# Kernel optimization log

Hardware: AMD Instinct MI355X
Metric: run time of the kernel (lower is better)

Reference implementation:

```python
import jax, jax.numpy as jnp
import numpy as np
import math

B, L, CIN = 16, 1024, 14
T = 256            # num_tokens
H = 2 * T          # S4 channel width
N = 32             # S4 state size (d_state)
E = 128            # embedding_dim
DEPTH = 6
BETA0, BETA1 = 1e-4, 2e-2


def conv1x1(W, b, x):
    # W: [O, C], b: [O], x: [B, C, L] -> [B, O, L]
    return jnp.einsum('oc,bcl->bol', W, x) + b[None, :, None]


def layernorm_c(x, g, b):
    # normalize over channel dim of [B, C, L]
    mu = jnp.mean(x, axis=1, keepdims=True)
    var = jnp.mean((x - mu) ** 2, axis=1, keepdims=True)
    return (x - mu) * jax.lax.rsqrt(var + 1e-5) * g[None, :, None] + b[None, :, None]


def s4d(u, log_dt, logA_re, A_im, C_re, C_im, D):
    # Standard S4D: diagonal SSM, ZOH-ish discretization, FFT depthwise conv.
    # u: [B, H, L]
    Lq = u.shape[-1]
    dt = jnp.exp(log_dt)                       # [H]
    A = -jnp.exp(logA_re) + 1j * A_im          # [H, N]
    dtA = A * dt[:, None]                      # [H, N]
    C = (C_re + 1j * C_im) * (jnp.exp(dtA) - 1.0) / A
    V = jnp.exp(dtA[:, :, None] * jnp.arange(Lq, dtype=jnp.float32))  # [H, N, L]
    K = 2.0 * jnp.einsum('hn,hnl->hl', C, V).real                    # [H, L]
    nfft = 2 * Lq
    y = jnp.fft.irfft(jnp.fft.rfft(u, n=nfft) * jnp.fft.rfft(K, n=nfft)[None], n=nfft)[..., :Lq]
    return y + D[None, :, None] * u


def setup_inputs() -> dict:
    key = jax.random.key(0)
    ks = iter(jax.random.split(key, 64))
    nrm = lambda shape, s=1.0: jax.random.normal(next(ks), shape, jnp.float32) * s
    inp = {}
    inp['x'] = nrm((B, L, CIN))
    inp['t'] = jax.random.uniform(next(ks), (B,), jnp.float32, 1e-3, 1.0)
    # diffusion embedding
    inp['gfp_W'] = nrm((E // 2,), 30.0)
    inp['emb_w1'] = nrm((E, E), E ** -0.5); inp['emb_b1'] = jnp.zeros((E,), jnp.float32)
    inp['emb_w2'] = nrm((E, E), E ** -0.5); inp['emb_b2'] = jnp.zeros((E,), jnp.float32)
    # top-level projections
    inp['in_w'] = nrm((T, CIN), CIN ** -0.5); inp['in_b'] = jnp.zeros((T,), jnp.float32)
    inp['out1_w'] = nrm((T, T), T ** -0.5); inp['out1_b'] = jnp.zeros((T,), jnp.float32)
    inp['out2_w'] = nrm((CIN, T), T ** -0.5); inp['out2_b'] = jnp.zeros((CIN,), jnp.float32)
    # per-block params (stacked over depth)
    inp['dp_w'] = nrm((DEPTH, T, E), E ** -0.5); inp['dp_b'] = jnp.zeros((DEPTH, T), jnp.float32)
    inp['ip_w'] = nrm((DEPTH, H, T), T ** -0.5); inp['ip_b'] = jnp.zeros((DEPTH, H), jnp.float32)
    inp['op_w'] = nrm((DEPTH, H, T), T ** -0.5); inp['op_b'] = jnp.zeros((DEPTH, H), jnp.float32)
    # S4D params: [DEPTH, 2, H, ...] (two S4 layers per block)
    lo, hi = math.log(1e-3), math.log(1e-1)
    inp['s4_log_dt'] = jax.random.uniform(next(ks), (DEPTH, 2, H), jnp.float32, lo, hi)
    inp['s4_logA_re'] = jnp.full((DEPTH, 2, H, N), math.log(0.5), jnp.float32)
    inp['s4_A_im'] = jnp.broadcast_to(math.pi * jnp.arange(N, dtype=jnp.float32), (DEPTH, 2, H, N)).copy()
    inp['s4_C_re'] = nrm((DEPTH, 2, H, N), 0.5 ** 0.5)
    inp['s4_C_im'] = nrm((DEPTH, 2, H, N), 0.5 ** 0.5)
    inp['s4_D'] = nrm((DEPTH, 2, H))
    inp['ln_g'] = jnp.ones((DEPTH, 2, H), jnp.float32)
    inp['ln_b'] = jnp.zeros((DEPTH, 2, H), jnp.float32)
    return inp


def reference(x, t, gfp_W, emb_w1, emb_b1, emb_w2, emb_b2, in_w, in_b,
              out1_w, out1_b, out2_w, out2_b, dp_w, dp_b, ip_w, ip_b,
              op_w, op_b, s4_log_dt, s4_logA_re, s4_A_im, s4_C_re, s4_C_im,
              s4_D, ln_g, ln_b):
    xt = jnp.swapaxes(x, -1, -2)  # [B, CIN, L]
    # Gaussian Fourier projection + MLP (SiLU)
    xp = t[:, None] * gfp_W[None, :] * (2.0 * math.pi)
    emb = jnp.concatenate([jnp.sin(xp), jnp.cos(xp)], axis=-1)        # [B, E]
    emb = jax.nn.silu(emb @ emb_w1.T + emb_b1)
    emb = jax.nn.silu(emb @ emb_w2.T + emb_b2)
    h = conv1x1(in_w, in_b, xt)                                       # [B, T, L]
    skip_sum = jnp.zeros_like(h)
    for d in range(DEPTH):
        y = h + (emb @ dp_w[d].T + dp_b[d])[:, :, None]
        y = conv1x1(ip_w[d], ip_b[d], y)                              # [B, H, L]
        y = s4d(y, s4_log_dt[d, 0], s4_logA_re[d, 0], s4_A_im[d, 0], s4_C_re[d, 0], s4_C_im[d, 0], s4_D[d, 0])
        y = layernorm_c(y, ln_g[d, 0], ln_b[d, 0])
        y = s4d(y, s4_log_dt[d, 1], s4_logA_re[d, 1], s4_A_im[d, 1], s4_C_re[d, 1], s4_C_im[d, 1], s4_D[d, 1])
        y = layernorm_c(y, ln_g[d, 1], ln_b[d, 1])
        gate, filt = jnp.split(y, 2, axis=1)
        y = jax.nn.sigmoid(gate) * jnp.tanh(filt)                     # [B, T, L]
        y = conv1x1(op_w[d], op_b[d], y)                              # [B, H, L]
        res, skip = jnp.split(y, 2, axis=1)
        h = (h + res) / math.sqrt(2.0)
        skip_sum = skip_sum + skip
    z = skip_sum / math.sqrt(float(DEPTH))
    z = jax.nn.relu(conv1x1(out1_w, out1_b, z))
    z = conv1x1(out2_w, out2_b, z)                                    # [B, CIN, L]
    beta = BETA0 + t * (BETA1 - BETA0)                                # linear schedule
    z = z / jnp.sqrt(beta)[:, None, None]
    return jnp.swapaxes(z, -1, -2)                                    # [B, L, CIN]
```

## Files before the change

### kernel.cpp

```cpp
#include <hip/hip_runtime.h>

#define BB     16
#define LLEN   1024
#define CINN   14
#define TSZ    256
#define HSZ    512
#define NST    32
#define ESZ    128
#define NDEPTH 6
#define QHN    (HSZ*NST)

#define RS2 0.70710678118654752f
#define IS6 0.40824829046386302f

typedef unsigned short u16;
typedef unsigned int   u32;
typedef _Float16 f16;
typedef __attribute__((ext_vector_type(2)))  _Float16 f16x2;
typedef __attribute__((ext_vector_type(4)))  _Float16 f16x4;
typedef __attribute__((ext_vector_type(8)))  _Float16 f16x8;
typedef __attribute__((ext_vector_type(16))) float    f32x16;

#define OFF_WIP   0u
#define OFF_WOP   393216u
#define OFF_LAMP  786432u
#define OFF_WO1   1181696u
#define OFF_BB    1214464u
#define OFF_Y16   5388288u
#define OFF_HT    9582592u
#define OFF_GT    11679744u
#define OFF_ST    13776896u
#define OFF_ZT    15874048u
#define OFF_MEAN  17971200u
#define OFF_RSTD  17987584u
#define OFF_MATS  18003968u
#define WS_FLOATS 55752704u

#define MATS_PER_LAYER ((size_t)512*12288)

__device__ __forceinline__ void gload_lds16(const void* g, void* l){
  __builtin_amdgcn_global_load_lds(
      (const __attribute__((address_space(1))) unsigned int*)g,
      (__attribute__((address_space(3))) unsigned int*)(unsigned int)(unsigned long long)l,
      16, 0, 0);
}

__device__ __forceinline__ size_t swz_idx(int b, int l, int g){
  return ((((size_t)b*4 + (g>>3))*1024 + l)*8 + ((g&7) ^ (l&7)))*8;
}

__global__ __launch_bounds__(256) void build_kernel(const float* __restrict__ log_dt,
                                                    const float* __restrict__ logA,
                                                    const float* __restrict__ Aim,
                                                    const float* __restrict__ Cre,
                                                    const float* __restrict__ Cim,
                                                    const float* __restrict__ Dd,
                                                    float2* __restrict__ lamP,
                                                    f16* __restrict__ mats){
  __shared__ float Pre[65][33];
  __shared__ float Pim[65][33];
  __shared__ float Kk[64];
  __shared__ float Kpart[4][64];
  __shared__ float2 Lm[32];
  __shared__ float2 Cc[32];
  int bid = blockIdx.x;
  int q   = bid >> 9;
  int h   = bid & 511;
  int tid = threadIdx.x;
  if (tid < 32){
    int n = tid;
    int gid = q*QHN + h*NST + n;
    float dt  = expf(log_dt[q*HSZ + h]);
    float are = -expf(logA[gid]);
    float aim = Aim[gid];
    float dre = are*dt, dim = aim*dt;
    float e   = expf(dre);
    float lre = e*cosf(dim), lim = e*sinf(dim);
    float nre = lre - 1.f, nim = lim;
    float invden = 1.f/(are*are + aim*aim);
    float tre = (nre*are + nim*aim)*invden;
    float tim = (nim*are - nre*aim)*invden;
    float cr = Cre[gid], ci = Cim[gid];
    Lm[n] = make_float2(lre, lim);
    Cc[n] = make_float2(2.f*(cr*tre - ci*tim), 2.f*(cr*tim + ci*tre));
    float pr = lre, pi = lim;
#pragma unroll
    for (int i=0;i<6;i++){ float t2 = pr*pr - pi*pi; pi = 2.f*pr*pi; pr = t2; }
    lamP[gid] = make_float2(pr, pi);
  }
  __syncthreads();
  int n  = tid & 31;
  int pg = tid >> 5;
  {
    float2 l = Lm[n];
    float ar=l.x, ai=l.y;
#pragma unroll
    for (int i=0;i<3;i++){ float t2 = ar*ar - ai*ai; ai = 2.f*ar*ai; ar = t2; }
    float br=1.f, bi=0.f;
    for (int i=0;i<pg;i++){ float t2 = br*ar - bi*ai; bi = br*ai + bi*ar; br = t2; }
    float pr=br, pi=bi;
#pragma unroll
    for (int i=0;i<8;i++){
      Pre[8*pg+i][n] = pr; Pim[8*pg+i][n] = pi;
      float t2 = pr*l.x - pi*l.y; pi = pr*l.y + pi*l.x; pr = t2;
    }
    if (pg == 7){ Pre[64][n] = pr; Pim[64][n] = pi; }
  }
  __syncthreads();
  {
    int m = tid & 63, p2 = tid >> 6;
    float s = 0.f;
#pragma unroll
    for (int n2=p2*8; n2<p2*8+8; n2++){
      float2 c_ = Cc[n2];
      s += c_.x*Pre[m][n2] - c_.y*Pim[m][n2];
    }
    Kpart[p2][m] = s;
  }
  __syncthreads();
  if (tid < 64) Kk[tid] = Kpart[0][tid]+Kpart[1][tid]+Kpart[2][tid]+Kpart[3][tid];
  __syncthreads();
  float Kdiag = Kk[0] + Dd[q*HSZ + h];
  f16* base = mats + (size_t)bid*12288;
#pragma unroll
  for (int jj=0; jj<6; jj++){
    int job = jj*256 + tid;
    int mat = job >> 9;
    int rem = job & 511;
    int m = rem & 63;
    int g = rem >> 6;
    f16x8 vals;
    if (mat == 0){
#pragma unroll
      for (int j8=0;j8<8;j8++){
        int k = g*8 + j8;
        float v = (m > k) ? Kk[m-k] : ((m == k) ? Kdiag : 0.f);
        vals[j8] = (f16)v;
      }
    } else if (mat == 1){
      int n2 = m >> 1; int im = m & 1;
#pragma unroll
      for (int j8=0;j8<8;j8++){
        int k = g*8 + j8; int p = 63 - k;
        vals[j8] = (f16)(im ? Pim[p][n2] : Pre[p][n2]);
      }
    } else {
#pragma unroll
      for (int j8=0;j8<8;j8++){
        int k = g*8 + j8; int n2 = k >> 1;
        float2 c_ = Cc[n2];
        float pr = Pre[m+1][n2], pi = Pim[m+1][n2];
        float re  = c_.x*pr - c_.y*pi;
        float imv = c_.x*pi + c_.y*pr;
        vals[j8] = (f16)((k & 1) ? -imv : re);
      }
    }
    *(f16x8*)(base + mat*4096 + (g*64 + m)*8) = vals;
  }
}

__global__ __launch_bounds__(256) void embdpe_bb(const float* __restrict__ t, const float* __restrict__ gw,
                                                 const float* __restrict__ w1, const float* __restrict__ b1,
                                                 const float* __restrict__ w2, const float* __restrict__ b2,
                                                 const float* __restrict__ dw, const float* __restrict__ db,
                                                 const float* __restrict__ ipw, const float* __restrict__ ipb,
                                                 float* __restrict__ bbp){
  __shared__ float e0[128], e1[128], e2[128];
  __shared__ float dpe[256];
  int bid = blockIdx.x;
  int d = bid >> 4, b = bid & 15;
  int tid = threadIdx.x;
  float tb = t[b];
  if (tid < 64){
    float xp = tb * gw[tid] * 6.283185307179586f;
    e0[tid]    = sinf(xp);
    e0[tid+64] = cosf(xp);
  }
  __syncthreads();
  if (tid < 128){
    float a = b1[tid];
    const float* wr = w1 + tid*128;
    for (int i=0;i<128;i++) a = fmaf(e0[i], wr[i], a);
    e1[tid] = a / (1.f + __expf(-a));
  }
  __syncthreads();
  if (tid < 128){
    float a2 = b2[tid];
    const float* wr = w2 + tid*128;
    for (int i=0;i<128;i++) a2 = fmaf(e1[i], wr[i], a2);
    e2[tid] = a2 / (1.f + __expf(-a2));
  }
  __syncthreads();
  {
    const float* wp = dw + (size_t)(d*TSZ + tid)*ESZ;
    float a = db[d*TSZ + tid];
    for (int e=0;e<128;e++) a = fmaf(e2[e], wp[e], a);
    dpe[tid] = a;
  }
  __syncthreads();
#pragma unroll
  for (int r=0;r<2;r++){
    int m = r*256 + tid;
    const float* wp = ipw + (size_t)(d*HSZ + m)*TSZ;
    float a = ipb[d*HSZ + m];
    for (int e=0;e<256;e++) a = fmaf(dpe[e], wp[e], a);
    bbp[(size_t)(d*BB + b)*HSZ + m] = a;
  }
}

__global__ __launch_bounds__(256) void prep_wts(const float* __restrict__ x,  const float* __restrict__ inw,
                                                const float* __restrict__ inb,
                                                const float* __restrict__ ipw, const float* __restrict__ opw,
                                                const float* __restrict__ o1w,
                                                f16* __restrict__ WfIP, f16* __restrict__ WfOP,
                                                f16* __restrict__ WfO1, f16* __restrict__ hT){
  __shared__ __align__(16) char SMEM[49152];
  int bid = blockIdx.x;
  int tid = threadIdx.x;
  if (bid < 256){
    float* ws  = (float*)SMEM;
    float* bs2 = (float*)(SMEM + 14336);
    f16*  TT   = (f16*)(SMEM + 15360);
#pragma unroll
    for (int c=0;c<14;c++) ws[tid*14+c] = inw[tid*14+c];
    bs2[tid] = inb[tid];
    __syncthreads();
    int b  = bid >> 4;
    int l0 = (bid & 15) * 64;
    int ll = tid & 63;
    int tq = tid >> 6;
    float xv[14];
    const float* xp = x + (size_t)(b*LLEN + l0 + ll)*CINN;
#pragma unroll
    for (int c=0;c<14;c++) xv[c] = xp[c];
    for (int tt=tq*64; tt<tq*64+64; tt++){
      float a = bs2[tt];
#pragma unroll
      for (int c=0;c<14;c++) a = fmaf(ws[tt*14+c], xv[c], a);
      TT[ll*264 + tt] = (f16)a;
    }
    __syncthreads();
#pragma unroll
    for (int i=0;i<8;i++){
      int job = i*256 + tid;
      int l2 = job >> 5, gi = job & 31;
      f16x8 hv = *(const f16x8*)(TT + l2*264 + gi*8);
      *(f16x8*)(hT + swz_idx(b, l0 + l2, gi)) = hv;
    }
  } else {
    int gid = (bid - 256)*256 + tid;
    const float* src; f16* dst; float scale = 1.f;
    if (gid < 98304){
      int d = gid >> 14, rem = gid & 16383, r = rem >> 5, g = rem & 31;
      src = ipw + ((size_t)(d*512 + r))*256 + g*8;
      dst = WfIP + (size_t)d*131072 + (((g>>3)*512 + r)*8 + ((g&7)^(r&7)))*8;
    } else if (gid < 196608){
      int g2 = gid - 98304;
      int d = g2 >> 14, rem = g2 & 16383, r = rem >> 5, g = rem & 31;
      src = opw + ((size_t)(d*512 + r))*256 + g*8;
      dst = WfOP + (size_t)d*131072 + (((g>>3)*512 + r)*8 + ((g&7)^(r&7)))*8;
    } else {
      int g3 = gid - 196608;
      int r = g3 >> 5, g = g3 & 31;
      src = o1w + (size_t)r*256 + g*8;
      dst = WfO1 + (((g>>3)*256 + r)*8 + ((g&7)^(r&7)))*8;
      scale = IS6;
    }
    float4 u0 = *(const float4*)src;
    float4 u1 = *(const float4*)(src+4);
    f16x8 hv;
    hv[0]=(f16)(u0.x*scale); hv[1]=(f16)(u0.y*scale); hv[2]=(f16)(u0.z*scale); hv[3]=(f16)(u0.w*scale);
    hv[4]=(f16)(u1.x*scale); hv[5]=(f16)(u1.y*scale); hv[6]=(f16)(u1.z*scale); hv[7]=(f16)(u1.w*scale);
    *(f16x8*)dst = hv;
  }
}

template<int MODE>
__global__ __launch_bounds__(256) void gemm_k(const f16* __restrict__ Wf, const float* __restrict__ bias,
                                              const f16* __restrict__ XT,
                                              f16* __restrict__ Y16o,
                                              f16* __restrict__ hT16, f16* __restrict__ sT16, int first){
  __shared__ __align__(16) f16 sm[17408];
  f16* As = sm;
  f16* Bs = sm + 8192;
  int tid = threadIdx.x;
  int lane = tid & 63;
  int wv = tid >> 6;
  int n_blk = blockIdx.x * 128;
  int m_blk = blockIdx.y * 128;
  int bz = blockIdx.z;
  const int M = (MODE==2) ? 256 : 512;
  int wm = (wv & 1) * 64;
  int wn = (wv >> 1) * 64;

  f32x16 acc[2][2];
#pragma unroll
  for (int mi=0;mi<2;mi++)
#pragma unroll
    for (int ni=0;ni<2;ni++)
#pragma unroll
      for (int r=0;r<16;r++) acc[mi][ni][r] = 0.f;

  for (int kt=0; kt<4; kt++){
    const f16* asrc = Wf + ((size_t)kt*M + m_blk)*64 + tid*8;
    const f16* bsrc = XT + ((size_t)(bz*4 + kt)*1024 + n_blk)*64 + tid*8;
#pragma unroll
    for (int i=0;i<4;i++){
      gload_lds16(asrc + i*2048, As + (i*256 + wv*64)*8);
      gload_lds16(bsrc + i*2048, Bs + (i*256 + wv*64)*8);
    }
    __syncthreads();
#pragma unroll
    for (int ks=0; ks<4; ks++){
      int q = lane >> 5;
      int gk = ks*2 + q;
      f16x8 af[2], bf[2];
#pragma unroll
      for (int mi=0; mi<2; mi++){
        int m = wm + mi*32 + (lane & 31);
        af[mi] = *(const f16x8*)(As + (m*8 + (gk ^ (m&7)))*8);
      }
#pragma unroll
      for (int ni=0; ni<2; ni++){
        int n = wn + ni*32 + (lane & 31);
        bf[ni] = *(const f16x8*)(Bs + (n*8 + (gk ^ (n&7)))*8);
      }
#pragma unroll
      for (int mi=0; mi<2; mi++)
#pragma unroll
        for (int ni=0; ni<2; ni++)
          acc[mi][ni] = __builtin_amdgcn_mfma_f32_32x32x16_f16(af[mi], bf[ni], acc[mi][ni], 0, 0, 0);
    }
    __syncthreads();
  }

  int q = lane >> 5;
  if (MODE == 0){
#pragma unroll
    for (int mi=0;mi<2;mi++)
#pragma unroll
      for (int ni=0;ni<2;ni++){
        int col_l = wn + ni*32 + (lane & 31);
#pragma unroll
        for (int r=0;r<16;r++){
          int row_l = wm + mi*32 + (r&3) + 8*(r>>2) + 4*q;
          float v = acc[mi][ni][r] + bias[bz*HSZ + m_blk + row_l];
          sm[row_l*136 + col_l] = (f16)v;
        }
      }
    __syncthreads();
#pragma unroll
    for (int i=0;i<8;i++){
      int job = i*256 + tid;
      int rr = job >> 4, c8 = job & 15;
      f16x8 hv = *(const f16x8*)(sm + rr*136 + c8*8);
      *(f16x8*)(Y16o + ((size_t)bz*HSZ + m_blk + rr)*LLEN + n_blk + c8*8) = hv;
    }
  } else if (MODE == 2){
#pragma unroll
    for (int mi=0;mi<2;mi++)
#pragma unroll
      for (int ni=0;ni<2;ni++){
        int col_l = wn + ni*32 + (lane & 31);
#pragma unroll
        for (int r=0;r<16;r++){
          int row_l = wm + mi*32 + (r&3) + 8*(r>>2) + 4*q;
          float v = fmaxf(acc[mi][ni][r] + bias[m_blk + row_l], 0.f);
          sm[col_l*136 + row_l] = (f16)v;
        }
      }
    __syncthreads();
#pragma unroll
    for (int i=0;i<8;i++){
      int job = i*256 + tid;
      int n = job >> 4, m8 = job & 15;
      f16x8 hv = *(const f16x8*)(sm + n*136 + m8*8);
      *(f16x8*)(Y16o + ((size_t)bz*LLEN + n_blk + n)*TSZ + m_blk + m8*8) = hv;
    }
  } else {
    int isRes = (blockIdx.y < 2);
    f16* dst = isRes ? hT16 : sT16;
    int gbase = isRes ? (m_blk >> 3) : ((m_blk - TSZ) >> 3);
    int doLoad = isRes || !first;
    if (doLoad){
#pragma unroll
      for (int i=0;i<8;i++){
        int job = i*256 + tid;
        int n = job >> 4, m8 = job & 15;
        f16x8 hv = *(const f16x8*)(dst + swz_idx(bz, n_blk + n, gbase + m8));
        *(f16x8*)(sm + n*136 + m8*8) = hv;
      }
      __syncthreads();
    }
#pragma unroll
    for (int mi=0;mi<2;mi++)
#pragma unroll
      for (int ni=0;ni<2;ni++){
        int col_l = wn + ni*32 + (lane & 31);
#pragma unroll
        for (int r=0;r<16;r++){
          int row_l = wm + mi*32 + (r&3) + 8*(r>>2) + 4*q;
          float v = acc[mi][ni][r] + bias[m_blk + row_l];
          if (isRes){
            float old = (float)sm[col_l*136 + row_l];
            sm[col_l*136 + row_l] = (f16)((old + v)*RS2);
          } else if (first){
            sm[col_l*136 + row_l] = (f16)v;
          } else {
            float old = (float)sm[col_l*136 + row_l];
            sm[col_l*136 + row_l] = (f16)(old + v);
          }
        }
      }
    __syncthreads();
#pragma unroll
    for (int i=0;i<8;i++){
      int job = i*256 + tid;
      int n = job >> 4, m8 = job & 15;
      f16x8 hv = *(const f16x8*)(sm + n*136 + m8*8);
      *(f16x8*)(dst + swz_idx(bz, n_blk + n, gbase + m8)) = hv;
    }
  }
}

template<int LN>
__global__ __launch_bounds__(128) void s4_mfma(const f16* __restrict__ matsq,
                                               const float2* __restrict__ lamPq,
                                               const f16* u, f16* y,
                                               const float* __restrict__ meanp,
                                               const float* __restrict__ rstdp,
                                               const float* __restrict__ gp,
                                               const float* __restrict__ btp){
  __shared__ f16 Ubuf[64*72];
  __shared__ f16 ZSbuf[64*72];

  int tid  = threadIdx.x;
  int w    = tid >> 6;
  int lane = tid & 63;
  int q    = lane >> 5;
  int colL = lane & 31;
  int h  = blockIdx.x & 511;
  int bq = blockIdx.x >> 9;
  int b0 = bq*4;

  float gv = 0.f, bv = 0.f;
  if (LN){ gv = gp[h]; bv = btp[h]; }

  const f16* matT = matsq + (size_t)h*12288;
  const f16* matV = matT + 4096;
  const f16* matE = matT + 8192;

#pragma unroll
  for (int i=0;i<4;i++){
    int fidx = i*64 + lane;
    int row = fidx >> 7;
    int l   = (fidx & 127)*8;
    int b   = b0 + 2*w + row;
    f16x8 hv = *(const f16x8*)(u + ((size_t)b*HSZ + h)*LLEN + l);
    if (LN){
      float4 m0 = *(const float4*)(meanp + b*LLEN + l);
      float4 m1 = *(const float4*)(meanp + b*LLEN + l + 4);
      float4 r0 = *(const float4*)(rstdp + b*LLEN + l);
      float4 r1 = *(const float4*)(rstdp + b*LLEN + l + 4);
      float mm[8] = {m0.x,m0.y,m0.z,m0.w,m1.x,m1.y,m1.z,m1.w};
      float rr[8] = {r0.x,r0.y,r0.z,r0.w,r1.x,r1.y,r1.z,r1.w};
#pragma unroll
      for (int e=0;e<8;e++)
        hv[e] = (f16)(((float)hv[e] - mm[e])*rr[e]*gv + bv);
    }
    int col = (2*w + row)*16 + (l >> 6);
    *(f16x8*)(Ubuf + col*72 + (l & 63)) = hv;
  }
  __syncthreads();

  int strip = w*32;

  {
    f32x16 zacc[2];
#pragma unroll
    for (int mt=0;mt<2;mt++)
#pragma unroll
      for (int r=0;r<16;r++) zacc[mt][r] = 0.f;
#pragma unroll
    for (int kt=0; kt<4; kt++){
      int kg = kt*2 + q;
      f16x8 bfrag = *(const f16x8*)(Ubuf + (strip+colL)*72 + kg*8);
#pragma unroll
      for (int mt=0; mt<2; mt++){
        f16x8 afrag = *(const f16x8*)(matV + ((size_t)(kg*64 + mt*32 + colL))*8);
        zacc[mt] = __builtin_amdgcn_mfma_f32_32x32x16_f16(afrag, bfrag, zacc[mt], 0, 0, 0);
      }
    }
#pragma unroll
    for (int mt=0;mt<2;mt++)
#pragma unroll
      for (int rg=0;rg<4;rg++){
        int st0 = mt*32 + rg*8 + q*4;
        f16x4 zp;
        zp[0]=(f16)zacc[mt][rg*4+0]; zp[1]=(f16)zacc[mt][rg*4+1];
        zp[2]=(f16)zacc[mt][rg*4+2]; zp[3]=(f16)zacc[mt][rg*4+3];
        *(f16x4*)(ZSbuf + (strip+colL)*72 + st0) = zp;
      }
  }
  __syncthreads();

  {
    int n  = lane & 31;
    int colb = (2*w + (lane>>5))*16;
    float2 l64 = lamPq[h*NST + n];
    f16x2 zv[16];
#pragma unroll
    for (int c=0;c<16;c++)
      zv[c] = *(f16x2*)(ZSbuf + (colb + c)*72 + 2*n);
    float Sre = 0.f, Sim = 0.f;
#pragma unroll
    for (int c=0;c<16;c++){
      float zr = (float)zv[c][0], zi = (float)zv[c][1];
      f16x2 sp_; sp_[0] = (f16)Sre; sp_[1] = (f16)Sim;
      zv[c] = sp_;
      float nr = fmaf(l64.x, Sre, fmaf(-l64.y, Sim, zr));
      float ni = fmaf(l64.x, Sim, fmaf( l64.y, Sre, zi));
      Sre = nr; Sim = ni;
    }
#pragma unroll
    for (int c=0;c<16;c++)
      *(f16x2*)(ZSbuf + (colb + c)*72 + 2*n) = zv[c];
  }
  __syncthreads();

  f32x16 yacc[2];
#pragma unroll
  for (int mt=0;mt<2;mt++)
#pragma unroll
    for (int r=0;r<16;r++) yacc[mt][r] = 0.f;
#pragma unroll
  for (int kt=0; kt<4; kt++){
    int kg = kt*2 + q;
    f16x8 bu = *(const f16x8*)(Ubuf  + (strip+colL)*72 + kg*8);
    f16x8 bs = *(const f16x8*)(ZSbuf + (strip+colL)*72 + kg*8);
#pragma unroll
    for (int mt=0; mt<2; mt++){
      f16x8 aT = *(const f16x8*)(matT + ((size_t)(kg*64 + mt*32 + colL))*8);
      yacc[mt] = __builtin_amdgcn_mfma_f32_32x32x16_f16(aT, bu, yacc[mt], 0, 0, 0);
    }
#pragma unroll
    for (int mt=0; mt<2; mt++){
      f16x8 aE = *(const f16x8*)(matE + ((size_t)(kg*64 + mt*32 + colL))*8);
      yacc[mt] = __builtin_amdgcn_mfma_f32_32x32x16_f16(aE, bs, yacc[mt], 0, 0, 0);
    }
  }
  __syncthreads();

#pragma unroll
  for (int mt=0;mt<2;mt++)
#pragma unroll
    for (int rg=0;rg<4;rg++){
      int j0 = mt*32 + rg*8 + q*4;
      f16x4 yv;
      yv[0]=(f16)yacc[mt][rg*4+0]; yv[1]=(f16)yacc[mt][rg*4+1];
      yv[2]=(f16)yacc[mt][rg*4+2]; yv[3]=(f16)yacc[mt][rg*4+3];
      *(f16x4*)(ZSbuf + (strip+colL)*72 + j0) = yv;
    }
  __syncthreads();
#pragma unroll
  for (int i=0;i<4;i++){
    int fidx = i*64 + lane;
    int row = fidx >> 7;
    int l   = (fidx & 127)*8;
    int b   = b0 + 2*w + row;
    int col = (2*w + row)*16 + (l >> 6);
    f16x8 hv = *(const f16x8*)(ZSbuf + col*72 + (l & 63));
    *(f16x8*)(y + ((size_t)b*HSZ + h)*LLEN + l) = hv;
  }
}

__global__ __launch_bounds__(256) void ln_stats(const f16* __restrict__ in,
                                                float* __restrict__ mean, float* __restrict__ rstd){
  __shared__ float rs[4][32];
  __shared__ float rq[4][32];
  int tid = threadIdx.x;
  int lg = tid & 3;
  int hb = tid >> 2;
  int w  = tid >> 6;
  int b  = blockIdx.x >> 5;
  int l0 = (blockIdx.x & 31) << 5;
  float s8[8], q8[8];
#pragma unroll
  for (int j=0;j<8;j++){ s8[j]=0.f; q8[j]=0.f; }
  const f16* basep = in + (size_t)(b*HSZ)*LLEN + l0 + lg*8;
#pragma unroll
  for (int i=0;i<8;i++){
    int h = hb + 64*i;
    f16x8 hv = *(const f16x8*)(basep + (size_t)h*LLEN);
#pragma unroll
    for (int j=0;j<8;j++){
      float v = (float)hv[j];
      s8[j] += v; q8[j] = fmaf(v,v,q8[j]);
    }
  }
#pragma unroll
  for (int d=4; d<64; d<<=1){
#pragma unroll
    for (int j=0;j<8;j++){
      s8[j] += __shfl_xor(s8[j], (unsigned)d);
      q8[j] += __shfl_xor(q8[j], (unsigned)d);
    }
  }
  if (((tid>>2) & 15) == 0){
#pragma unroll
    for (int j=0;j<8;j++){
      rs[w][lg*8+j] = s8[j];
      rq[w][lg*8+j] = q8[j];
    }
  }
  __syncthreads();
  if (tid < 32){
    float S = rs[0][tid]+rs[1][tid]+rs[2][tid]+rs[3][tid];
    float Q = rq[0][tid]+rq[1][tid]+rq[2][tid]+rq[3][tid];
    float mn = S * (1.f/HSZ);
    float var = Q * (1.f/HSZ) - mn*mn;
    mean[b*LLEN + l0 + tid] = mn;
    rstd[b*LLEN + l0 + tid] = rsqrtf(var + 1e-5f);
  }
}

__global__ __launch_bounds__(256) void ln_gate_kernel(const f16* __restrict__ in, f16* __restrict__ gT,
                                                      const float* __restrict__ g, const float* __restrict__ bt){
  __shared__ float rs[4][32];
  __shared__ float rq[4][32];
  __shared__ float mbuf[32], rbuf[32];
  __shared__ f16 gbuf[32*264];
  int tid = threadIdx.x;
  int lg = tid & 3;
  int w  = tid >> 6;
  int b  = blockIdx.x >> 5;
  int l0 = (blockIdx.x & 31) << 5;
  {
    int hb = tid >> 2;
    float s8[8], q8[8];
#pragma unroll
    for (int j=0;j<8;j++){ s8[j]=0.f; q8[j]=0.f; }
    const f16* basep = in + (size_t)(b*HSZ)*LLEN + l0 + lg*8;
#pragma unroll
    for (int i=0;i<8;i++){
      int h = hb + 64*i;
      f16x8 hv = *(const f16x8*)(basep + (size_t)h*LLEN);
#pragma unroll
      for (int j=0;j<8;j++){
        float v = (float)hv[j];
        s8[j] += v; q8[j] = fmaf(v,v,q8[j]);
      }
    }
#pragma unroll
    for (int d=4; d<64; d<<=1){
#pragma unroll
      for (int j=0;j<8;j++){
        s8[j] += __shfl_xor(s8[j], (unsigned)d);
        q8[j] += __shfl_xor(q8[j], (unsigned)d);
      }
    }
    if (((tid>>2) & 15) == 0){
#pragma unroll
      for (int j=0;j<8;j++){
        rs[w][lg*8+j] = s8[j];
        rq[w][lg*8+j] = q8[j];
      }
    }
  }
  __syncthreads();
  if (tid < 32){
    float S = rs[0][tid]+rs[1][tid]+rs[2][tid]+rs[3][tid];
    float Q = rq[0][tid]+rq[1][tid]+rq[2][tid]+rq[3][tid];
    float mn = S * (1.f/HSZ);
    float var = Q * (1.f/HSZ) - mn*mn;
    mbuf[tid] = mn;
    rbuf[tid] = rsqrtf(var + 1e-5f);
  }
  __syncthreads();
  {
    int tq = tid >> 2;
    float mloc[8], rloc[8];
#pragma unroll
    for (int j=0;j<8;j++){ mloc[j]=mbuf[lg*8+j]; rloc[j]=rbuf[lg*8+j]; }
    const f16* basep = in + (size_t)(b*HSZ)*LLEN + l0 + lg*8;
#pragma unroll
    for (int i=0;i<4;i++){
      int t = tq + 64*i;
      f16x8 av = *(const f16x8*)(basep + (size_t)t*LLEN);
      f16x8 fv = *(const f16x8*)(basep + (size_t)(t+256)*LLEN);
      float ga = g[t], ba = bt[t], gf = g[t+256], bf2 = bt[t+256];
#pragma unroll
      for (int j=0;j<8;j++){
        float a = ((float)av[j] - mloc[j])*rloc[j]*ga + ba;
        float f = ((float)fv[j] - mloc[j])*rloc[j]*gf + bf2;
        float sg = 1.f/(1.f+__expf(-a));
        float th = 1.f - 2.f/(__expf(2.f*f)+1.f);
        gbuf[(lg*8+j)*264 + t] = (f16)(sg*th);
      }
    }
  }
  __syncthreads();
#pragma unroll
  for (int i=0;i<4;i++){
    int job = i*256 + tid;
    int ll = job >> 5, gi = job & 31;
    f16x8 hv = *(const f16x8*)(gbuf + ll*264 + gi*8);
    *(f16x8*)(gT + swz_idx(b, l0 + ll, gi)) = hv;
  }
}

__global__ __launch_bounds__(256) void out2_kernel(const float* __restrict__ w2, const float* __restrict__ b2,
                                                   const float* __restrict__ t, const f16* __restrict__ zT,
                                                   float* __restrict__ outp){
  __shared__ f16 zt[64*264];
  __shared__ float wsm[14*256];
  __shared__ float part[64][4][16];
  __shared__ float bs[14];
  int tid = threadIdx.x;
#pragma unroll
  for (int c=0;c<14;c++) wsm[c*256+tid] = w2[c*256+tid];
  if (tid < 14) bs[tid] = b2[tid];
  int b = blockIdx.x >> 4;
  int l0 = (blockIdx.x & 15) * 64;
#pragma unroll
  for (int i=0;i<8;i++){
    int job = i*256 + tid;
    int ll = job >> 5, g8 = (job & 31)*8;
    f16x8 hv = *(const f16x8*)(zT + ((size_t)b*LLEN + l0 + ll)*TSZ + g8);
    *(f16x8*)(zt + ll*264 + g8) = hv;
  }
  __syncthreads();
  int l = tid >> 2;
  int g = tid & 3;
  float acc[14];
#pragma unroll
  for (int c=0;c<14;c++) acc[c]=0.f;
  for (int k=0;k<64;k++){
    float zv = (float)zt[l*264 + g*64 + k];
#pragma unroll
    for (int c=0;c<14;c++) acc[c] = fmaf(wsm[c*256 + g*64 + k], zv, acc[c]);
  }
#pragma unroll
  for (int c=0;c<14;c++) part[l][g][c] = acc[c];
  __syncthreads();
  if (g == 0){
    float tb = t[b];
    float scale = rsqrtf(1e-4f + tb*(2e-2f - 1e-4f));
    float* op = outp + (size_t)(b*LLEN + l0 + l)*CINN;
#pragma unroll
    for (int c=0;c<14;c++)
      op[c] = (part[l][0][c]+part[l][1][c]+part[l][2][c]+part[l][3][c] + bs[c])*scale;
  }
}

extern "C" void kernel_launch(void* const* d_in, const int* in_sizes, int n_in,
                              void* d_out, int out_size, void* d_ws, size_t ws_size,
                              hipStream_t stream) {
  (void)in_sizes; (void)n_in; (void)out_size;
  if (ws_size < (size_t)WS_FLOATS * 4) return;

  const float* x      = (const float*)d_in[0];
  const float* t      = (const float*)d_in[1];
  const float* gfpW   = (const float*)d_in[2];
  const float* ew1    = (const float*)d_in[3];
  const float* eb1    = (const float*)d_in[4];
  const float* ew2    = (const float*)d_in[5];
  const float* eb2    = (const float*)d_in[6];
  const float* in_w   = (const float*)d_in[7];
  const float* in_b   = (const float*)d_in[8];
  const float* out1_w = (const float*)d_in[9];
  const float* out1_b = (const float*)d_in[10];
  const float* out2_w = (const float*)d_in[11];
  const float* out2_b = (const float*)d_in[12];
  const float* dp_w   = (const float*)d_in[13];
  const float* dp_b   = (const float*)d_in[14];
  const float* ip_w   = (const float*)d_in[15];
  const float* ip_b   = (const float*)d_in[16];
  const float* op_w   = (const float*)d_in[17];
  const float* op_b   = (const float*)d_in[18];
  const float* log_dt = (const float*)d_in[19];
  const float* logA   = (const float*)d_in[20];
  const float* Aim    = (const float*)d_in[21];
  const float* Cre    = (const float*)d_in[22];
  const float* Cim    = (const float*)d_in[23];
  const float* s4D    = (const float*)d_in[24];
  const float* ln_g   = (const float*)d_in[25];
  const float* ln_b   = (const float*)d_in[26];
  float* out = (float*)d_out;
  float* ws = (float*)d_ws;

  f16*    WfIP = (f16*)(ws + OFF_WIP);
  f16*    WfOP = (f16*)(ws + OFF_WOP);
  float2* lamP = (float2*)(ws + OFF_LAMP);
  f16*    WfO1 = (f16*)(ws + OFF_WO1);
  float*  bbp  = ws + OFF_BB;
  f16*    y16  = (f16*)(ws + OFF_Y16);
  f16*    hT16 = (f16*)(ws + OFF_HT);
  f16*    gT16 = (f16*)(ws + OFF_GT);
  f16*    sT16 = (f16*)(ws + OFF_ST);
  f16*    zT16 = (f16*)(ws + OFF_ZT);
  float*  meanb = ws + OFF_MEAN;
  float*  rstdb = ws + OFF_RSTD;
  f16*    mats = (f16*)(ws + OFF_MATS);

  build_kernel<<<6144,256,0,stream>>>(log_dt, logA, Aim, Cre, Cim, s4D, lamP, mats);
  embdpe_bb<<<96,256,0,stream>>>(t, gfpW, ew1, eb1, ew2, eb2, dp_w, dp_b, ip_w, ip_b, bbp);
  prep_wts<<<1056,256,0,stream>>>(x, in_w, in_b, ip_w, op_w, out1_w,
                                  WfIP, WfOP, WfO1, hT16);

  for (int d=0; d<NDEPTH; d++){
    int q0 = d*2, q1 = d*2+1;
    gemm_k<0><<<dim3(8,4,16),256,0,stream>>>(WfIP + (size_t)d*131072, bbp + (size_t)d*BB*HSZ,
                                             hT16, y16, nullptr, nullptr, 0);
    s4_mfma<0><<<2048,128,0,stream>>>(mats + (size_t)q0*MATS_PER_LAYER, lamP + (size_t)q0*QHN,
                                      y16, y16, nullptr, nullptr, nullptr, nullptr);
    ln_stats<<<512,256,0,stream>>>(y16, meanb, rstdb);
    s4_mfma<1><<<2048,128,0,stream>>>(mats + (size_t)q1*MATS_PER_LAYER, lamP + (size_t)q1*QHN,
                                      y16, y16, meanb, rstdb, ln_g + q0*HSZ, ln_b + q0*HSZ);
    ln_gate_kernel<<<512,256,0,stream>>>(y16, gT16, ln_g + q1*HSZ, ln_b + q1*HSZ);
    gemm_k<1><<<dim3(8,4,16),256,0,stream>>>(WfOP + (size_t)d*131072, op_b + d*HSZ,
                                             gT16, nullptr, hT16, sT16, (d==0)?1:0);
  }
  gemm_k<2><<<dim3(8,2,16),256,0,stream>>>(WfO1, out1_b, sT16, zT16, nullptr, nullptr, 0);
  out2_kernel<<<256,256,0,stream>>>(out2_w, out2_b, t, zT16, out);
}
```

Before: 649.8 us.

## Double-buffer GEMM LDS tiles, merge embedding kernel, cache LN input in LDS

```diff
diff --git a/kernel.cpp b/kernel.cpp
--- a/kernel.cpp
+++ b/kernel.cpp
@@ -159,61 +159,18 @@
   }
 }
 
-__global__ __launch_bounds__(256) void embdpe_bb(const float* __restrict__ t, const float* __restrict__ gw,
-                                                 const float* __restrict__ w1, const float* __restrict__ b1,
-                                                 const float* __restrict__ w2, const float* __restrict__ b2,
-                                                 const float* __restrict__ dw, const float* __restrict__ db,
-                                                 const float* __restrict__ ipw, const float* __restrict__ ipb,
-                                                 float* __restrict__ bbp){
-  __shared__ float e0[128], e1[128], e2[128];
-  __shared__ float dpe[256];
-  int bid = blockIdx.x;
-  int d = bid >> 4, b = bid & 15;
-  int tid = threadIdx.x;
-  float tb = t[b];
-  if (tid < 64){
-    float xp = tb * gw[tid] * 6.283185307179586f;
-    e0[tid]    = sinf(xp);
-    e0[tid+64] = cosf(xp);
-  }
-  __syncthreads();
-  if (tid < 128){
-    float a = b1[tid];
-    const float* wr = w1 + tid*128;
-    for (int i=0;i<128;i++) a = fmaf(e0[i], wr[i], a);
-    e1[tid] = a / (1.f + __expf(-a));
-  }
-  __syncthreads();
-  if (tid < 128){
-    float a2 = b2[tid];
-    const float* wr = w2 + tid*128;
-    for (int i=0;i<128;i++) a2 = fmaf(e1[i], wr[i], a2);
-    e2[tid] = a2 / (1.f + __expf(-a2));
-  }
-  __syncthreads();
-  {
-    const float* wp = dw + (size_t)(d*TSZ + tid)*ESZ;
-    float a = db[d*TSZ + tid];
-    for (int e=0;e<128;e++) a = fmaf(e2[e], wp[e], a);
-    dpe[tid] = a;
-  }
-  __syncthreads();
-#pragma unroll
-  for (int r=0;r<2;r++){
-    int m = r*256 + tid;
-    const float* wp = ipw + (size_t)(d*HSZ + m)*TSZ;
-    float a = ipb[d*HSZ + m];
-    for (int e=0;e<256;e++) a = fmaf(dpe[e], wp[e], a);
-    bbp[(size_t)(d*BB + b)*HSZ + m] = a;
-  }
-}
-
 __global__ __launch_bounds__(256) void prep_wts(const float* __restrict__ x,  const float* __restrict__ inw,
                                                 const float* __restrict__ inb,
                                                 const float* __restrict__ ipw, const float* __restrict__ opw,
                                                 const float* __restrict__ o1w,
+                                                const float* __restrict__ t,  const float* __restrict__ gw,
+                                                const float* __restrict__ w1, const float* __restrict__ b1,
+                                                const float* __restrict__ w2, const float* __restrict__ b2,
+                                                const float* __restrict__ dw, const float* __restrict__ db,
+                                                const float* __restrict__ ipb,
                                                 f16* __restrict__ WfIP, f16* __restrict__ WfOP,
-                                                f16* __restrict__ WfO1, f16* __restrict__ hT){
+                                                f16* __restrict__ WfO1, f16* __restrict__ hT,
+                                                float* __restrict__ bbp){
   __shared__ __align__(16) char SMEM[49152];
   int bid = blockIdx.x;
   int tid = threadIdx.x;
@@ -247,7 +204,7 @@
       f16x8 hv = *(const f16x8*)(TT + l2*264 + gi*8);
       *(f16x8*)(hT + swz_idx(b, l0 + l2, gi)) = hv;
     }
-  } else {
+  } else if (bid < 1056){
     int gid = (bid - 256)*256 + tid;
     const float* src; f16* dst; float scale = 1.f;
     if (gid < 98304){
@@ -272,6 +229,49 @@
     hv[0]=(f16)(u0.x*scale); hv[1]=(f16)(u0.y*scale); hv[2]=(f16)(u0.z*scale); hv[3]=(f16)(u0.w*scale);
     hv[4]=(f16)(u1.x*scale); hv[5]=(f16)(u1.y*scale); hv[6]=(f16)(u1.z*scale); hv[7]=(f16)(u1.w*scale);
     *(f16x8*)dst = hv;
+  } else {
+    float* e0  = (float*)SMEM;
+    float* e1  = (float*)(SMEM + 512);
+    float* e2  = (float*)(SMEM + 1024);
+    float* dpe = (float*)(SMEM + 1536);
+    int idx = bid - 1056;
+    int d = idx >> 4, b = idx & 15;
+    float tb = t[b];
+    if (tid < 64){
+      float xp = tb * gw[tid] * 6.283185307179586f;
+      e0[tid]    = sinf(xp);
+      e0[tid+64] = cosf(xp);
+    }
+    __syncthreads();
+    if (tid < 128){
+      float a = b1[tid];
+      const float* wr = w1 + tid*128;
+      for (int i=0;i<128;i++) a = fmaf(e0[i], wr[i], a);
+      e1[tid] = a / (1.f + __expf(-a));
+    }
+    __syncthreads();
+    if (tid < 128){
+      float a2 = b2[tid];
+      const float* wr = w2 + tid*128;
+      for (int i=0;i<128;i++) a2 = fmaf(e1[i], wr[i], a2);
+      e2[tid] = a2 / (1.f + __expf(-a2));
+    }
+    __syncthreads();
+    {
+      const float* wp = dw + (size_t)(d*TSZ + tid)*ESZ;
+      float a = db[d*TSZ + tid];
+      for (int e=0;e<128;e++) a = fmaf(e2[e], wp[e], a);
+      dpe[tid] = a;
+    }
+    __syncthreads();
+#pragma unroll
+    for (int r=0;r<2;r++){
+      int m = r*256 + tid;
+      const float* wp = ipw + (size_t)(d*HSZ + m)*TSZ;
+      float a = ipb[d*HSZ + m];
+      for (int e=0;e<256;e++) a = fmaf(dpe[e], wp[e], a);
+      bbp[(size_t)(d*BB + b)*HSZ + m] = a;
+    }
   }
 }
 
@@ -280,9 +280,7 @@
                                               const f16* __restrict__ XT,
                                               f16* __restrict__ Y16o,
                                               f16* __restrict__ hT16, f16* __restrict__ sT16, int first){
-  __shared__ __align__(16) f16 sm[17408];
-  f16* As = sm;
-  f16* Bs = sm + 8192;
+  __shared__ __align__(16) f16 sm[32768];
   int tid = threadIdx.x;
   int lane = tid & 63;
   int wv = tid >> 6;
@@ -301,15 +299,30 @@
 #pragma unroll
       for (int r=0;r<16;r++) acc[mi][ni][r] = 0.f;
 
+  const f16* asrc0 = Wf + (size_t)m_blk*64 + tid*8;
+  const f16* bsrc0 = XT + ((size_t)(bz*4)*1024 + n_blk)*64 + tid*8;
+
+#pragma unroll
+  for (int i=0;i<4;i++){
+    gload_lds16(asrc0 + i*2048, sm + (i*256 + wv*64)*8);
+    gload_lds16(bsrc0 + i*2048, sm + 8192 + (i*256 + wv*64)*8);
+  }
+  __syncthreads();
+
+#pragma unroll
   for (int kt=0; kt<4; kt++){
-    const f16* asrc = Wf + ((size_t)kt*M + m_blk)*64 + tid*8;
-    const f16* bsrc = XT + ((size_t)(bz*4 + kt)*1024 + n_blk)*64 + tid*8;
-#pragma unroll
-    for (int i=0;i<4;i++){
-      gload_lds16(asrc + i*2048, As + (i*256 + wv*64)*8);
-      gload_lds16(bsrc + i*2048, Bs + (i*256 + wv*64)*8);
-    }
-    __syncthreads();
+    if (kt < 3){
+      int nb = ((kt+1)&1)*16384;
+      const f16* an = asrc0 + (size_t)(kt+1)*M*64;
+      const f16* bn = bsrc0 + (size_t)(kt+1)*1024*64;
+#pragma unroll
+      for (int i=0;i<4;i++){
+        gload_lds16(an + i*2048, sm + nb + (i*256 + wv*64)*8);
+        gload_lds16(bn + i*2048, sm + nb + 8192 + (i*256 + wv*64)*8);
+      }
+    }
+    const f16* As = sm + (kt&1)*16384;
+    const f16* Bs = As + 8192;
 #pragma unroll
     for (int ks=0; ks<4; ks++){
       int q = lane >> 5;
@@ -629,6 +642,7 @@
   __shared__ float rs[4][32];
   __shared__ float rq[4][32];
   __shared__ float mbuf[32], rbuf[32];
+  __shared__ __align__(16) f16 ybuf[512*40];
   __shared__ f16 gbuf[32*264];
   int tid = threadIdx.x;
   int lg = tid & 3;
@@ -645,6 +659,7 @@
     for (int i=0;i<8;i++){
       int h = hb + 64*i;
       f16x8 hv = *(const f16x8*)(basep + (size_t)h*LLEN);
+      *(f16x8*)(ybuf + h*40 + lg*8) = hv;
 #pragma unroll
       for (int j=0;j<8;j++){
         float v = (float)hv[j];
@@ -682,12 +697,11 @@
     float mloc[8], rloc[8];
 #pragma unroll
     for (int j=0;j<8;j++){ mloc[j]=mbuf[lg*8+j]; rloc[j]=rbuf[lg*8+j]; }
-    const f16* basep = in + (size_t)(b*HSZ)*LLEN + l0 + lg*8;
 #pragma unroll
     for (int i=0;i<4;i++){
       int t = tq + 64*i;
-      f16x8 av = *(const f16x8*)(basep + (size_t)t*LLEN);
-      f16x8 fv = *(const f16x8*)(basep + (size_t)(t+256)*LLEN);
+      f16x8 av = *(const f16x8*)(ybuf + t*40 + lg*8);
+      f16x8 fv = *(const f16x8*)(ybuf + (t+256)*40 + lg*8);
       float ga = g[t], ba = bt[t], gf = g[t+256], bf2 = bt[t+256];
 #pragma unroll
       for (int j=0;j<8;j++){
@@ -804,9 +818,9 @@
   f16*    mats = (f16*)(ws + OFF_MATS);
 
   build_kernel<<<6144,256,0,stream>>>(log_dt, logA, Aim, Cre, Cim, s4D, lamP, mats);
-  embdpe_bb<<<96,256,0,stream>>>(t, gfpW, ew1, eb1, ew2, eb2, dp_w, dp_b, ip_w, ip_b, bbp);
-  prep_wts<<<1056,256,0,stream>>>(x, in_w, in_b, ip_w, op_w, out1_w,
-                                  WfIP, WfOP, WfO1, hT16);
+  prep_wts<<<1152,256,0,stream>>>(x, in_w, in_b, ip_w, op_w, out1_w,
+                                  t, gfpW, ew1, eb1, ew2, eb2, dp_w, dp_b, ip_b,
+                                  WfIP, WfOP, WfO1, hT16, bbp);
 
   for (int d=0; d<NDEPTH; d++){
     int q0 = d*2, q1 = d*2+1;
```

Measured after the change: 665.9 us. 2.5% more time.
